# Optimization experiments

Hardware: AMD Instinct MI355X
Metric: run time of the kernel (lower is better)

Reference implementation:

```python
import jax, jax.numpy as jnp
from jax import lax
import numpy as np

# NOTE: the original module calls an opaque CUDA 'approximate dot-product' conv kernel.
# Its backward uses EXACT conv2d gradients for input/weight, so the reference forward
# math is the exact conv2d the kernel approximates. `approximate` is a learned scalar
# controlling the hardware approximation level; it does not change the exact-math output.

STRIDE = 1
PAD = (1, 1)  # (padH, padW)


def setup_inputs() -> dict:
    key = jax.random.key(0)
    k1, k2, k3 = jax.random.split(key, 3)
    B, Cin, H, W = 32, 128, 56, 56
    Cout, K = 256, 3
    x = jax.random.normal(k1, (B, Cin, H, W), dtype=jnp.float32)
    # weight init: uniform(-1, 1) per reset_parameters
    weight = jax.random.uniform(k2, (Cout, Cin, K, K), dtype=jnp.float32, minval=-1.0, maxval=1.0)
    fan_in = Cin * K * K
    bound = 1.0 / np.sqrt(fan_in)
    bias = jax.random.uniform(k3, (Cout,), dtype=jnp.float32, minval=-bound, maxval=bound)
    approximate = jnp.ones((1,), dtype=jnp.float32)
    return {"x": x, "weight": weight, "bias": bias, "approximate": approximate}


def reference(x, weight, bias, approximate):
    # Exact conv2d, NCHW input, OIHW kernel. `approximate` controls only the
    # hardware approximation level in the original CUDA kernel.
    out = lax.conv_general_dilated(
        x, weight,
        window_strides=(STRIDE, STRIDE),
        padding=((PAD[0], PAD[0]), (PAD[1], PAD[1])),
        dimension_numbers=("NCHW", "OIHW", "NCHW"),
    )
    return out + bias.reshape(1, -1, 1, 1)
```

## Files before the change

kernel.cpp:

```cpp
#include <hip/hip_runtime.h>


typedef __attribute__((ext_vector_type(8))) short short8;
typedef __attribute__((ext_vector_type(4))) float floatx4;

typedef __attribute__((address_space(1))) const void* gas_ptr;
typedef __attribute__((address_space(3))) void* las_ptr;

__device__ static inline void gl2lds16(const void* g, void* l) {
    __builtin_amdgcn_global_load_lds((gas_ptr)g, (las_ptr)l, 16, 0, 0);
}

__device__ static inline float bf2f(unsigned short u) {
    union { unsigned int i; float f; } x; x.i = ((unsigned int)u) << 16; return x.f;
}
__device__ static inline unsigned short f2bf(float f) {
    union { float f; unsigned int i; } x; x.f = f;
    unsigned int r = (x.i + 0x7FFFu + ((x.i >> 16) & 1u)) >> 16;
    return (unsigned short)r;
}

__device__ static inline bool wave_detect_bf16(const unsigned int* __restrict__ p) {
    const int lane = threadIdx.x & 63;
    int cnt = 0;
#pragma unroll
    for (int r = 0; r < 4; ++r) {
        unsigned int w = p[r * 64 + lane];
        unsigned short lo = (unsigned short)(w & 0xFFFFu);
        int e = (lo >> 7) & 0xFF;
        bool plaus = (lo == 0) || (e >= 96 && e <= 144);
        cnt += (int)__popcll(__ballot(plaus));
    }
    return cnt >= 205;
}

__global__ void wt_repack(const void* __restrict__ wsrc,
                          unsigned short* __restrict__ wt) {
    const bool isbf = wave_detect_bf16((const unsigned int*)wsrc);
    int idx = blockIdx.x * 256 + threadIdx.x;
    int ci  = idx & 127;
    int co  = (idx >> 7) & 255;
    int off = idx >> 15;
    size_t s = (size_t)(co * 128 + ci) * 9 + off;
    float v = isbf ? bf2f(((const unsigned short*)wsrc)[s])
                   : ((const float*)wsrc)[s];
    wt[idx] = f2bf(v);
}

__global__ __launch_bounds__(256) void x_repack(
    const void* __restrict__ xsrc, unsigned short* __restrict__ xp) {
    __shared__ unsigned short tile[56 * 130];
    const int bh  = blockIdx.x;
    const int b   = bh / 58, hp = bh - b * 58;
    const int tid = threadIdx.x;
    unsigned short* row = xp + (size_t)(b * 58 + hp) * 58 * 128;
    if (hp == 0 || hp == 57) {
        uint4 z; z.x = z.y = z.z = z.w = 0u;
        uint4* r = (uint4*)row;
        for (int t = tid; t < 928; t += 256) r[t] = z;
        return;
    }
    const bool isbf = wave_detect_bf16((const unsigned int*)xsrc);
    const int h = hp - 1;
    if (isbf) {
        const unsigned short* xs =
            (const unsigned short*)xsrc + (size_t)b * 128 * 3136 + h * 56;
#pragma unroll
        for (int it = 0; it < 7; ++it) {
            int idx = it * 256 + tid;
            int ci = idx / 14, w4 = idx - ci * 14;
            ushort4 v = *(const ushort4*)(xs + (size_t)ci * 3136 + w4 * 4);
            tile[(w4 * 4 + 0) * 130 + ci] = v.x;
            tile[(w4 * 4 + 1) * 130 + ci] = v.y;
            tile[(w4 * 4 + 2) * 130 + ci] = v.z;
            tile[(w4 * 4 + 3) * 130 + ci] = v.w;
        }
    } else {
        const float* xs = (const float*)xsrc + (size_t)b * 128 * 3136 + h * 56;
#pragma unroll
        for (int it = 0; it < 7; ++it) {
            int idx = it * 256 + tid;
            int ci = idx / 14, w4 = idx - ci * 14;
            float4 v = *(const float4*)(xs + (size_t)ci * 3136 + w4 * 4);
            tile[(w4 * 4 + 0) * 130 + ci] = f2bf(v.x);
            tile[(w4 * 4 + 1) * 130 + ci] = f2bf(v.y);
            tile[(w4 * 4 + 2) * 130 + ci] = f2bf(v.z);
            tile[(w4 * 4 + 3) * 130 + ci] = f2bf(v.w);
        }
    }
    __syncthreads();
#pragma unroll
    for (int it = 0; it < 4; ++it) {
        int k = it * 256 + tid;
        if (k >= 928) break;
        int wq = k >> 4, cc = k & 15;
        uint4 v;
        if (wq == 0 || wq == 57) { v.x = v.y = v.z = v.w = 0u; }
        else {
            const unsigned short* p = &tile[(wq - 1) * 130 + cc * 8];
            union { unsigned short s[8]; uint4 u; } pk;
#pragma unroll
            for (int j = 0; j < 8; ++j) pk.s[j] = p[j];
            v = pk.u;
        }
        *(uint4*)(row + wq * 128 + cc * 8) = v;
    }
}

__global__ __launch_bounds__(384) void conv_mfma(
    const unsigned short* __restrict__ xp,
    const unsigned short* __restrict__ wt,
    const void* __restrict__ bias,
    void* __restrict__ out,
    const void* __restrict__ xorig)
{
    __shared__ __align__(16) char lds[49152];
    __shared__ unsigned ready[3];
    __shared__ unsigned freed[3];
    const int tid   = threadIdx.x;
    const int lane  = tid & 63;
    const int wv    = tid >> 6;
    const int ntile = blockIdx.x;
    const int mtile = blockIdx.y;

    if (tid < 3) { ready[tid] = 0u; freed[tid] = 0u; }
    __syncthreads();

    if (wv >= 4) {
        const int pid = wv - 4;
        const int srp = lane >> 2;
        const int clg = (lane & 3) ^ ((lane >> 3) & 3);
        const unsigned short* aB = wt + (mtile * 128 + srp) * 128 + clg * 8;
        size_t bRow[8];
#pragma unroll
        for (int i = 0; i < 8; ++i) {
            const int n = ntile * 128 + i * 16 + srp;
            const int b = n / 3136, s2 = n - b * 3136;
            const int h = s2 / 56,  w = s2 - h * 56;
            bRow[i] = ((size_t)(b * 58 + h) * 58 + w) * 128 + clg * 8;
        }
        int bf_ = pid;
        for (int s = pid; s < 36; s += 2) {
            if (s >= 3) {
                const unsigned gate = 4u * (unsigned)(s / 3);
                while (__hip_atomic_load(&freed[bf_], __ATOMIC_ACQUIRE,
                                         __HIP_MEMORY_SCOPE_WORKGROUP) < gate)
                    __builtin_amdgcn_s_sleep(1);
            }
            char* buf = lds + bf_ * 16384;
            const int off = s >> 2, kb = (s & 3) << 5;
            const int dh = off / 3, dw = off - dh * 3;
            const int aoff = off * 32768 + kb;
            const int boff = (dh * 58 + dw) * 128 + kb;
#pragma unroll
            for (int i = 0; i < 8; ++i)
                gl2lds16(aB + i * 2048 + aoff, buf + i * 1024);
#pragma unroll
            for (int i = 0; i < 8; ++i)
                gl2lds16(xp + bRow[i] + boff, buf + 8192 + i * 1024);
            __builtin_amdgcn_s_waitcnt(0x3F70);
            if (lane == 0)
                __hip_atomic_store(&ready[bf_], (unsigned)(s + 1),
                                   __ATOMIC_RELEASE, __HIP_MEMORY_SCOPE_WORKGROUP);
            bf_ += 2; if (bf_ >= 3) bf_ -= 3;
        }
        return;
    }

    const bool isbf = wave_detect_bf16((const unsigned int*)xorig);
    const int mbase = (wv >> 1) * 64 + (lane & 15);
    const int nbase = (wv & 1) * 64 + (lane & 15);
    const int ph    = (lane >> 4) ^ (((lane & 15) >> 1) & 3);
    floatx4 acc[4][4] = {};

#pragma unroll 3
    for (int s = 0; s < 36; ++s) {
        const int bf_ = s % 3;
        while (__hip_atomic_load(&ready[bf_], __ATOMIC_ACQUIRE,
                                 __HIP_MEMORY_SCOPE_WORKGROUP) < (unsigned)(s + 1))
            ;
        const char* la = lds + bf_ * 16384;
        const char* lb = la + 8192;
        short8 af[4], bfr[4];
#pragma unroll
        for (int t = 0; t < 4; ++t) {
            af[t]  = *(const short8*)(la + (mbase + t * 16) * 64 + ph * 16);
            bfr[t] = *(const short8*)(lb + (nbase + t * 16) * 64 + ph * 16);
        }
#pragma unroll
        for (int i = 0; i < 4; ++i)
#pragma unroll
            for (int j = 0; j < 4; ++j)
                acc[i][j] = __builtin_amdgcn_mfma_f32_16x16x32_bf16(
                    af[i], bfr[j], acc[i][j], 0, 0, 0);
        if (lane == 0)
            __hip_atomic_fetch_add(&freed[bf_], 1u, __ATOMIC_RELEASE,
                                   __HIP_MEMORY_SCOPE_WORKGROUP);
    }

    const int q = lane >> 4;
#pragma unroll
    for (int j = 0; j < 4; ++j) {
        const int n = ntile * 128 + (wv & 1) * 64 + j * 16 + (lane & 15);
        const int b = n / 3136;
        const int s = n - b * 3136;
#pragma unroll
        for (int i = 0; i < 4; ++i) {
            const int co = mtile * 128 + (wv >> 1) * 64 + i * 16 + q * 4;
            float bv[4];
            if (isbf) {
                const ushort4 bb = *(const ushort4*)((const unsigned short*)bias + co);
                bv[0] = bf2f(bb.x); bv[1] = bf2f(bb.y);
                bv[2] = bf2f(bb.z); bv[3] = bf2f(bb.w);
            } else {
                const float4 bb = *(const float4*)((const float*)bias + co);
                bv[0] = bb.x; bv[1] = bb.y; bv[2] = bb.z; bv[3] = bb.w;
            }
#pragma unroll
            for (int r = 0; r < 4; ++r) {
                const float v = acc[i][j][r] + bv[r];
                const size_t o = (size_t)b * 802816 + (size_t)(co + r) * 3136 + s;
                if (isbf) ((unsigned short*)out)[o] = f2bf(v);
                else      ((float*)out)[o] = v;
            }
        }
    }
}

__global__ void conv_naive(const float* __restrict__ x,
                           const float* __restrict__ w,
                           const float* __restrict__ bias,
                           float* __restrict__ out) {
    long long i = (long long)blockIdx.x * 256 + threadIdx.x;
    if (i >= 25690112LL) return;
    int wo = (int)(i % 56); long long t = i / 56;
    int ho = (int)(t % 56); t /= 56;
    int co = (int)(t % 256); int b = (int)(t / 256);
    float acc = bias[co];
    for (int ci = 0; ci < 128; ++ci)
        for (int dh = 0; dh < 3; ++dh) {
            int hi = ho + dh - 1; if ((unsigned)hi >= 56u) continue;
            for (int dw = 0; dw < 3; ++dw) {
                int wi = wo + dw - 1; if ((unsigned)wi >= 56u) continue;
                acc += x[((size_t)(b * 128 + ci) * 56 + hi) * 56 + wi] *
                       w[((co * 128 + ci) * 3 + dh) * 3 + dw];
            }
        }
    out[i] = acc;
}

extern "C" void kernel_launch(void* const* d_in, const int* in_sizes, int n_in,
                              void* d_out, int out_size, void* d_ws, size_t ws_size,
                              hipStream_t stream) {
    const void* x    = d_in[0];
    const void* w    = d_in[1];
    const void* bias = d_in[2];

    const size_t xp_bytes = (size_t)32 * 58 * 58 * 128 * 2;
    const size_t wt_off   = xp_bytes;
    const size_t wt_bytes = (size_t)9 * 256 * 128 * 2;
    const size_t need     = wt_off + wt_bytes;

    if (ws_size >= need) {
        unsigned short* xp = (unsigned short*)d_ws;
        unsigned short* wt = (unsigned short*)((char*)d_ws + wt_off);
        x_repack<<<32 * 58, 256, 0, stream>>>(x, xp);
        wt_repack<<<1152, 256, 0, stream>>>(w, wt);
        dim3 grid(784, 2, 1);
        conv_mfma<<<grid, 384, 0, stream>>>(xp, wt, bias, d_out, x);
    } else {
        conv_naive<<<(25690112 + 255) / 256, 256, 0, stream>>>(
            (const float*)x, (const float*)w, (const float*)bias, (float*)d_out);
    }
}
```

Measured before the change: 227.9 us.

## Replace producer/consumer waves with 256x256 tile, 4-stage barrier-synced pipeline

Drops the producer-wave specialization and its LDS atomic ready/freed flags. All 8 waves now cooperatively prefetch a 256x256 output tile (all Cout at once) through a 4-deep LDS ring using global_load_lds, with barriers and s_setprio around the MFMA blocks. The larger tile raises operand reuse per LDS load and removes the spin-wait flag overhead. In exchange, 128KB of LDS limits each CU to one block, and the 392-block grid gives an uneven second wave across CUs.

Measured after the change: 216.9 us. -4.8%, faster.

```diff
diff --git a/kernel.cpp b/kernel.cpp
--- a/kernel.cpp
+++ b/kernel.cpp
@@ -107,119 +107,153 @@
     }
 }
 
-__global__ __launch_bounds__(384) void conv_mfma(
+__global__ __launch_bounds__(512, 2) void conv_mfma(
     const unsigned short* __restrict__ xp,
     const unsigned short* __restrict__ wt,
     const void* __restrict__ bias,
     void* __restrict__ out,
     const void* __restrict__ xorig)
 {
-    __shared__ __align__(16) char lds[49152];
-    __shared__ unsigned ready[3];
-    __shared__ unsigned freed[3];
+    __shared__ __align__(16) char lds[131072];
     const int tid   = threadIdx.x;
     const int lane  = tid & 63;
     const int wv    = tid >> 6;
     const int ntile = blockIdx.x;
-    const int mtile = blockIdx.y;
-
-    if (tid < 3) { ready[tid] = 0u; freed[tid] = 0u; }
-    __syncthreads();
-
-    if (wv >= 4) {
-        const int pid = wv - 4;
-        const int srp = lane >> 2;
-        const int clg = (lane & 3) ^ ((lane >> 3) & 3);
-        const unsigned short* aB = wt + (mtile * 128 + srp) * 128 + clg * 8;
-        size_t bRow[8];
-#pragma unroll
-        for (int i = 0; i < 8; ++i) {
-            const int n = ntile * 128 + i * 16 + srp;
-            const int b = n / 3136, s2 = n - b * 3136;
-            const int h = s2 / 56,  w = s2 - h * 56;
-            bRow[i] = ((size_t)(b * 58 + h) * 58 + w) * 128 + clg * 8;
-        }
-        int bf_ = pid;
-        for (int s = pid; s < 36; s += 2) {
-            if (s >= 3) {
-                const unsigned gate = 4u * (unsigned)(s / 3);
-                while (__hip_atomic_load(&freed[bf_], __ATOMIC_ACQUIRE,
-                                         __HIP_MEMORY_SCOPE_WORKGROUP) < gate)
-                    __builtin_amdgcn_s_sleep(1);
-            }
-            char* buf = lds + bf_ * 16384;
-            const int off = s >> 2, kb = (s & 3) << 5;
-            const int dh = off / 3, dw = off - dh * 3;
-            const int aoff = off * 32768 + kb;
-            const int boff = (dh * 58 + dw) * 128 + kb;
-#pragma unroll
-            for (int i = 0; i < 8; ++i)
-                gl2lds16(aB + i * 2048 + aoff, buf + i * 1024);
-#pragma unroll
-            for (int i = 0; i < 8; ++i)
-                gl2lds16(xp + bRow[i] + boff, buf + 8192 + i * 1024);
-            __builtin_amdgcn_s_waitcnt(0x3F70);
-            if (lane == 0)
-                __hip_atomic_store(&ready[bf_], (unsigned)(s + 1),
-                                   __ATOMIC_RELEASE, __HIP_MEMORY_SCOPE_WORKGROUP);
-            bf_ += 2; if (bf_ >= 3) bf_ -= 3;
-        }
-        return;
-    }
 
     const bool isbf = wave_detect_bf16((const unsigned int*)xorig);
-    const int mbase = (wv >> 1) * 64 + (lane & 15);
-    const int nbase = (wv & 1) * 64 + (lane & 15);
-    const int ph    = (lane >> 4) ^ (((lane & 15) >> 1) & 3);
-    floatx4 acc[4][4] = {};
-
-#pragma unroll 3
-    for (int s = 0; s < 36; ++s) {
-        const int bf_ = s % 3;
-        while (__hip_atomic_load(&ready[bf_], __ATOMIC_ACQUIRE,
-                                 __HIP_MEMORY_SCOPE_WORKGROUP) < (unsigned)(s + 1))
-            ;
-        const char* la = lds + bf_ * 16384;
-        const char* lb = la + 8192;
-        short8 af[4], bfr[4];
-#pragma unroll
-        for (int t = 0; t < 4; ++t) {
-            af[t]  = *(const short8*)(la + (mbase + t * 16) * 64 + ph * 16);
-            bfr[t] = *(const short8*)(lb + (nbase + t * 16) * 64 + ph * 16);
-        }
+
+    const bool isA = (wv < 4);
+    const int  clg = (lane & 3) ^ ((lane >> 3) & 3);
+    const int  rsub = lane >> 2;
+    unsigned sb[4]; int db[4];
+    if (isA) {
+#pragma unroll
+        for (int s = 0; s < 4; ++s) {
+            const int c  = (wv & 3) * 4 + s;
+            const int co = c * 16 + rsub;
+            sb[s] = (unsigned)(co * 256 + clg * 16);
+            db[s] = c * 1024;
+        }
+    } else {
+#pragma unroll
+        for (int s = 0; s < 4; ++s) {
+            const int c = (wv & 3) * 4 + s;
+            const int n = ntile * 256 + c * 16 + rsub;
+            const int b = n / 3136, rem = n - b * 3136;
+            const int hh = rem / 56, ww = rem - hh * 56;
+            sb[s] = (unsigned)((((b * 58 + hh) * 58 + ww) * 256) + clg * 16);
+            db[s] = 16384 + c * 1024;
+        }
+    }
+    const char* gbase = isA ? (const char*)wt : (const char*)xp;
+
+    auto hdelta = [&](int h) -> int {
+        const int off = h >> 2, q = h & 3;
+        if (isA) return off * 65536 + q * 64;
+        const int dh = off / 3, dw = off - dh * 3;
+        return (dh * 58 + dw) * 256 + q * 64;
+    };
+
+    const int fr = lane & 15;
+    const int ph = (lane >> 4) ^ ((fr >> 1) & 3);
+    const int wm = wv >> 2;
+    const int wn = wv & 3;
+    const int aOff = (wm * 128 + fr) * 64 + ph * 16;
+    const int bOff = 16384 + (wn * 64 + fr) * 64 + ph * 16;
+
+    floatx4 acc[8][4] = {};
+
+#pragma unroll
+    for (int h = 0; h < 3; ++h) {
+        char* lb = lds + (h & 3) * 32768;
+        const int d = hdelta(h);
+#pragma unroll
+        for (int s = 0; s < 4; ++s)
+            gl2lds16(gbase + sb[s] + d, lb + db[s]);
+    }
+    __builtin_amdgcn_s_waitcnt(0x3F78);
+    __builtin_amdgcn_s_barrier();
+
+#pragma unroll 4
+    for (int h = 0; h < 36; ++h) {
+        const char* la  = lds + (h & 3) * 32768;
+        char* sdst      = lds + ((h + 3) & 3) * 32768;
+        const int  dlt  = (h < 33) ? hdelta(h + 3) : 0;
+        short8 af[8], bf[4];
+
+#pragma unroll
+        for (int i = 0; i < 4; ++i)
+            af[i] = *(const short8*)(la + aOff + i * 1024);
+#pragma unroll
+        for (int j = 0; j < 4; ++j)
+            bf[j] = *(const short8*)(la + bOff + j * 1024);
+        if (h < 33) {
+            gl2lds16(gbase + sb[0] + dlt, sdst + db[0]);
+            gl2lds16(gbase + sb[1] + dlt, sdst + db[1]);
+        }
+        __builtin_amdgcn_s_barrier();
+        __builtin_amdgcn_s_setprio(1);
 #pragma unroll
         for (int i = 0; i < 4; ++i)
 #pragma unroll
             for (int j = 0; j < 4; ++j)
                 acc[i][j] = __builtin_amdgcn_mfma_f32_16x16x32_bf16(
-                    af[i], bfr[j], acc[i][j], 0, 0, 0);
-        if (lane == 0)
-            __hip_atomic_fetch_add(&freed[bf_], 1u, __ATOMIC_RELEASE,
-                                   __HIP_MEMORY_SCOPE_WORKGROUP);
-    }
-
-    const int q = lane >> 4;
+                    af[i], bf[j], acc[i][j], 0, 0, 0);
+        __builtin_amdgcn_s_setprio(0);
+        __builtin_amdgcn_s_barrier();
+
+#pragma unroll
+        for (int i = 0; i < 4; ++i)
+            af[4 + i] = *(const short8*)(la + aOff + (4 + i) * 1024);
+        if (h < 33) {
+            gl2lds16(gbase + sb[2] + dlt, sdst + db[2]);
+            gl2lds16(gbase + sb[3] + dlt, sdst + db[3]);
+        }
+        __builtin_amdgcn_s_barrier();
+        __builtin_amdgcn_s_setprio(1);
+#pragma unroll
+        for (int i = 0; i < 4; ++i)
+#pragma unroll
+            for (int j = 0; j < 4; ++j)
+                acc[4 + i][j] = __builtin_amdgcn_mfma_f32_16x16x32_bf16(
+                    af[4 + i], bf[j], acc[4 + i][j], 0, 0, 0);
+        __builtin_amdgcn_s_setprio(0);
+
+        if (h < 35) {
+            if (h <= 32)      __builtin_amdgcn_s_waitcnt(0x3F78);
+            else if (h == 33) __builtin_amdgcn_s_waitcnt(0x3F74);
+            else              __builtin_amdgcn_s_waitcnt(0x3F70);
+            __builtin_amdgcn_s_barrier();
+        }
+    }
+
+    const int q4 = (lane >> 4) << 2;
+    int nb[4], ns[4];
 #pragma unroll
     for (int j = 0; j < 4; ++j) {
-        const int n = ntile * 128 + (wv & 1) * 64 + j * 16 + (lane & 15);
-        const int b = n / 3136;
-        const int s = n - b * 3136;
-#pragma unroll
-        for (int i = 0; i < 4; ++i) {
-            const int co = mtile * 128 + (wv >> 1) * 64 + i * 16 + q * 4;
-            float bv[4];
-            if (isbf) {
-                const ushort4 bb = *(const ushort4*)((const unsigned short*)bias + co);
-                bv[0] = bf2f(bb.x); bv[1] = bf2f(bb.y);
-                bv[2] = bf2f(bb.z); bv[3] = bf2f(bb.w);
-            } else {
-                const float4 bb = *(const float4*)((const float*)bias + co);
-                bv[0] = bb.x; bv[1] = bb.y; bv[2] = bb.z; bv[3] = bb.w;
-            }
+        const int n = ntile * 256 + wn * 64 + j * 16 + fr;
+        nb[j] = n / 3136;
+        ns[j] = n - nb[j] * 3136;
+    }
+#pragma unroll
+    for (int i = 0; i < 8; ++i) {
+        const int co = wm * 128 + i * 16 + q4;
+        float bv[4];
+        if (isbf) {
+            const ushort4 bb = *(const ushort4*)((const unsigned short*)bias + co);
+            bv[0] = bf2f(bb.x); bv[1] = bf2f(bb.y);
+            bv[2] = bf2f(bb.z); bv[3] = bf2f(bb.w);
+        } else {
+            const float4 bb = *(const float4*)((const float*)bias + co);
+            bv[0] = bb.x; bv[1] = bb.y; bv[2] = bb.z; bv[3] = bb.w;
+        }
+#pragma unroll
+        for (int j = 0; j < 4; ++j) {
 #pragma unroll
             for (int r = 0; r < 4; ++r) {
                 const float v = acc[i][j][r] + bv[r];
-                const size_t o = (size_t)b * 802816 + (size_t)(co + r) * 3136 + s;
+                const size_t o = (size_t)nb[j] * 802816 +
+                                 (size_t)(co + r) * 3136 + ns[j];
                 if (isbf) ((unsigned short*)out)[o] = f2bf(v);
                 else      ((float*)out)[o] = v;
             }
@@ -266,8 +300,7 @@
         unsigned short* wt = (unsigned short*)((char*)d_ws + wt_off);
         x_repack<<<32 * 58, 256, 0, stream>>>(x, xp);
         wt_repack<<<1152, 256, 0, stream>>>(w, wt);
-        dim3 grid(784, 2, 1);
-        conv_mfma<<<grid, 384, 0, stream>>>(xp, wt, bias, d_out, x);
+        conv_mfma<<<dim3(392, 1, 1), 512, 0, stream>>>(xp, wt, bias, d_out, x);
     } else {
         conv_naive<<<(25690112 + 255) / 256, 256, 0, stream>>>(
             (const float*)x, (const float*)w, (const float*)bias, (float*)d_out);
```
